# Performance work log

Hardware: AMD Instinct MI355X
Metric: run time of the kernel (lower is better)

## Reference

```python
import jax, jax.numpy as jnp
import numpy as np

B, D, K, NC, R = 32768, 512, 64, 64, 8
TRANSPORT_EPS = 1e-3
TAU_MIN = 0.01
TAU_DENOM_MIN = 1e-3
SCALE = 0.02


def setup_inputs() -> dict:
    key = jax.random.key(0)
    ks = jax.random.split(key, 8)
    f = jnp.float32
    return {
        "z": jax.random.normal(ks[0], (B, D), f),
        "w_z": jax.random.normal(ks[1], (K, D), f) * SCALE,          # q_z_proj weight
        "b_z": jnp.zeros((K,), f),                                     # q_z_proj bias
        "g_out": jax.random.normal(ks[2], (R, K), f) * SCALE,         # q_gamma_out
        "g_u": jax.random.normal(ks[3], (R, D), f) * SCALE,           # q_gamma_u
        "g_v": jax.random.normal(ks[4], (R, D), f) * SCALE,           # q_gamma_v
        "chart_queries": jax.random.normal(ks[5], (NC, K), f) * SCALE,
        "w_t": jax.random.normal(ks[6], (K * K, D), f) * SCALE,      # transport_proj weight
    }


def reference(z, w_z, b_z, g_out, g_u, g_v, chart_queries, w_t):
    # query: linear + low-rank gamma term (z_u * z_v) @ g_out
    q = z @ w_z.T + b_z                                # [B, K]
    q = q + ((z @ g_u.T) * (z @ g_v.T)) @ g_out        # [B, K]

    # Wilson-line transport: Cayley transform of a skew-symmetric matrix
    skew = (z @ w_t.T).reshape(-1, K, K)               # [B, K, K]
    skew = 0.5 * (skew - jnp.swapaxes(skew, 1, 2))
    eye = (1.0 + TRANSPORT_EPS) * jnp.eye(K, dtype=z.dtype)
    u = jnp.linalg.solve(eye + 0.5 * skew, eye[None, :, :] - 0.5 * skew)  # [B, K, K]

    keys = jnp.einsum('bij,nj->bni', u, chart_queries)  # [B, NC, K]
    scores = jnp.einsum('bnk,bk->bn', keys, q)          # [B, NC]

    # metric-aware temperature
    r2 = jnp.sum(z * z, axis=-1)
    denom = jnp.maximum(1.0 - r2, TAU_DENOM_MIN)
    tau = jnp.maximum(jnp.sqrt(jnp.asarray(K, z.dtype)) * denom / 2.0, TAU_MIN)

    router_weights = jax.nn.softmax(scores / tau[:, None], axis=-1)
    K_chart = jnp.argmax(router_weights, axis=-1)
    return router_weights, K_chart
```

## Files before the change

### kernel.cpp

```cpp
#include <hip/hip_runtime.h>
#include <cstdint>
#include <cstddef>
#include <cmath>

#define B_N   32768
#define D_DIM 512
#define NC_N  64
#define NTRI  2016
#define NP    2176
#define Q0    2016
#define U0    2080
#define V0    2088
#define KP    1536
#define KT_N  24
#define TEPS  1e-3f
#define SC1   0x1.0p-22f

typedef unsigned short u16;
typedef _Float16 f16;
typedef __attribute__((ext_vector_type(8))) _Float16 f16x8;
typedef __attribute__((ext_vector_type(4))) float f32x4;
typedef __attribute__((ext_vector_type(2))) float f32x2;

__device__ __forceinline__ u16 h_of(float x) { f16 h = (f16)x; return *reinterpret_cast<u16*>(&h); }
__device__ __forceinline__ float f_of_h(u16 u) { f16 h = *reinterpret_cast<f16*>(&u); return (float)h; }
__device__ __forceinline__ float rdlane(float x, int k) {
    return __int_as_float(__builtin_amdgcn_readlane(__float_as_int(x), k));
}
__device__ __forceinline__ float frcp(float x) {
    float r = __builtin_amdgcn_rcpf(x);
    return r * fmaf(-x, r, 2.0f);
}

__device__ __forceinline__ void split2(float x, u16& h, u16& l) {
    float s = x * 2048.0f;
    h = h_of(s);
    l = h_of(s - f_of_h(h));
}

__global__ __launch_bounds__(256) void prep_w_kernel(
    const float* __restrict__ wt, const float* __restrict__ wz,
    const float* __restrict__ gu, const float* __restrict__ gv,
    u16* __restrict__ dst)
{
    int t = blockIdx.x * 256 + threadIdx.x;
    if (t >= NP * 128) return;
    int row = t >> 7;
    int c4  = (t & 127) << 2;
    float4 v = make_float4(0.f, 0.f, 0.f, 0.f);
    if (row < NTRI) {
        int p = row;
        int i = (int)((127.0 - sqrt(16129.0 - 8.0 * (double)p)) * 0.5);
        if (i < 0) i = 0; if (i > 62) i = 62;
        while (i > 0 && (i * (127 - i)) / 2 > p) --i;
        while (((i + 1) * (126 - i)) / 2 <= p) ++i;
        int j = p - (i * (127 - i)) / 2 + i + 1;
        float4 a = *(const float4*)(wt + (size_t)(j * 64 + i) * 512 + c4);
        float4 b = *(const float4*)(wt + (size_t)(i * 64 + j) * 512 + c4);
        v.x = 0.25f * (a.x - b.x);
        v.y = 0.25f * (a.y - b.y);
        v.z = 0.25f * (a.z - b.z);
        v.w = 0.25f * (a.w - b.w);
    }
    else if (row < U0)        v = *(const float4*)(wz + (size_t)(row - Q0) * 512 + c4);
    else if (row < V0)        v = *(const float4*)(gu + (size_t)(row - U0) * 512 + c4);
    else if (row < V0 + 8)    v = *(const float4*)(gv + (size_t)(row - V0) * 512 + c4);
    ushort4 hv, lv;
    split2(v.x, hv.x, lv.x); split2(v.y, hv.y, lv.y);
    split2(v.z, hv.z, lv.z); split2(v.w, hv.w, lv.w);
    u16* base = dst + (size_t)row * KP + c4;
    *(ushort4*)(base)        = hv;
    *(ushort4*)(base + 512)  = lv;
    *(ushort4*)(base + 1024) = hv;
}

__global__ __launch_bounds__(256) void prep_z_kernel(
    const float* __restrict__ z, u16* __restrict__ dst, int chunkStart, int CB)
{
    int t = blockIdx.x * 256 + threadIdx.x;
    if (t >= CB * 128) return;
    int row = t >> 7;
    int c4  = (t & 127) << 2;
    float4 v = *(const float4*)(z + (size_t)(chunkStart + row) * 512 + c4);
    ushort4 hv, lv;
    split2(v.x, hv.x, lv.x); split2(v.y, hv.y, lv.y);
    split2(v.z, hv.z, lv.z); split2(v.w, hv.w, lv.w);
    u16* base = dst + (size_t)row * KP + c4;
    *(ushort4*)(base)        = hv;
    *(ushort4*)(base + 512)  = hv;
    *(ushort4*)(base + 1024) = lv;
}

__global__ __launch_bounds__(256) void gemm_kernel(
    const u16* __restrict__ A, const u16* __restrict__ Bw, float* __restrict__ C)
{
    __shared__ alignas(16) u16 As[128 * 64];
    __shared__ alignas(16) u16 Bs[128 * 64];
    const int t    = threadIdx.x;
    const int lane = t & 63;
    const int w    = t >> 6;
    const int wr   = w >> 1, wc = w & 1;

    const int nwg = gridDim.x * gridDim.y;
    int flat = blockIdx.y * gridDim.x + blockIdx.x;
    if ((nwg & 7) == 0) {
        const int cpx = nwg >> 3;
        flat = (flat & 7) * cpx + (flat >> 3);
    }
    const int bx = flat % gridDim.x;
    const int by = flat / gridDim.x;
    const size_t m0 = (size_t)by * 128;
    const size_t n0 = (size_t)bx * 128;

    const char* Ab = (const char*)A  + (m0 + (size_t)(t >> 3)) * (KP * 2) + (size_t)(t & 7) * 16;
    const char* Bb = (const char*)Bw + (n0 + (size_t)(t >> 3)) * (KP * 2) + (size_t)(t & 7) * 16;
    char* AsB = (char*)&As[0];
    char* BsB = (char*)&Bs[0];

    f32x4 acc[4][4];
    #pragma unroll
    for (int i = 0; i < 4; ++i)
        #pragma unroll
        for (int j = 0; j < 4; ++j)
            acc[i][j] = (f32x4){0.f, 0.f, 0.f, 0.f};

    const int lr = lane & 15;
    const int lk = (lane >> 4) * 8;

    #pragma unroll 1
    for (int kt = 0; kt < KT_N; ++kt) {
        __syncthreads();
        const size_t koff = (size_t)kt * 128;
        #pragma unroll
        for (int cc = 0; cc < 4; ++cc) {
            __builtin_amdgcn_global_load_lds(
                (const __attribute__((address_space(1))) unsigned int*)(Ab + (size_t)cc * (32 * KP * 2) + koff),
                (__attribute__((address_space(3))) unsigned int*)(AsB + cc * 4096 + w * 1024),
                16, 0, 0);
            __builtin_amdgcn_global_load_lds(
                (const __attribute__((address_space(1))) unsigned int*)(Bb + (size_t)cc * (32 * KP * 2) + koff),
                (__attribute__((address_space(3))) unsigned int*)(BsB + cc * 4096 + w * 1024),
                16, 0, 0);
        }
        asm volatile("s_waitcnt vmcnt(0)" ::: "memory");
        __syncthreads();
        #pragma unroll
        for (int kk = 0; kk < 64; kk += 32) {
            f16x8 af[4], bf[4];
            #pragma unroll
            for (int i = 0; i < 4; ++i) {
                af[i] = *(const f16x8*)&As[(wr * 64 + i * 16 + lr) * 64 + kk + lk];
                bf[i] = *(const f16x8*)&Bs[(wc * 64 + i * 16 + lr) * 64 + kk + lk];
            }
            #pragma unroll
            for (int i = 0; i < 4; ++i)
                #pragma unroll
                for (int j = 0; j < 4; ++j)
                    acc[i][j] = __builtin_amdgcn_mfma_f32_16x16x32_f16(af[i], bf[j], acc[i][j], 0, 0, 0);
        }
    }
    const int fq = lane >> 4;
    const int fr = lane & 15;
    #pragma unroll
    for (int i = 0; i < 4; ++i) {
        #pragma unroll
        for (int j = 0; j < 4; ++j) {
            size_t crow = m0 + (size_t)(wr * 64 + i * 16 + fq * 4);
            size_t ccol = n0 + (size_t)(wc * 64 + j * 16 + fr);
            #pragma unroll
            for (int r = 0; r < 4; ++r)
                __builtin_nontemporal_store(acc[i][j][r] * SC1, &C[(crow + r) * NP + ccol]);
        }
    }
}

__global__ __launch_bounds__(256) void solve_kernel(
    const float* __restrict__ z, const float* __restrict__ bz,
    const float* __restrict__ gout, const float* __restrict__ cq,
    const float* __restrict__ G, float* __restrict__ rw, float* __restrict__ kc,
    int chunkStart)
{
    const int tid  = threadIdx.x;
    const int lane = tid & 63;
    const int smp  = tid >> 6;
    const int sl   = (blockIdx.x << 2) + smp;
    const size_t s = (size_t)chunkStart + sl;
    const float c  = 1.0f + TEPS;

    __shared__ alignas(16) float Vs[4][2048];

    const float* Grow = G + (size_t)sl * NP;

    const float4* G4 = (const float4*)Grow;
    float4* Vw = (float4*)&Vs[smp][0];
    #pragma unroll
    for (int it = 0; it < 8; ++it) {
        int idx = it * 64 + lane;
        if (idx < NTRI / 4) Vw[idx] = G4[idx];
    }

    const float4* zr = (const float4*)(z + s * 512);
    float4 za = zr[lane];
    float4 zb = zr[64 + lane];
    float r2 = za.x * za.x + za.y * za.y + za.z * za.z + za.w * za.w
             + zb.x * zb.x + zb.y * zb.y + zb.z * zb.z + zb.w * zb.w;
    #pragma unroll
    for (int o = 32; o; o >>= 1) r2 += __shfl_xor(r2, o);

    float qv = bz[lane] + Grow[Q0 + lane];
    #pragma unroll
    for (int r = 0; r < 8; ++r) {
        float a = Grow[U0 + r];
        float b = Grow[V0 + r];
        qv = fmaf(a * b, gout[r * 64 + lane], qv);
    }
    const float qorig = qv;

    const int ibase = (lane * (127 - lane)) / 2 - lane - 1;
    f32x2 m2[32];
    #pragma unroll
    for (int j = 0; j < 64; ++j) {
        const int jbase = (j * (127 - j)) / 2 - j - 1;
        int addr = (j > lane) ? (ibase + j) : (jbase + lane);
        addr = (j == lane) ? 0 : addr;
        float v = Vs[smp][addr];
        float val = (j > lane) ? v : -v;
        val = (j == lane) ? 0.0f : val;
        if (j & 1) m2[j >> 1].y = val; else m2[j >> 1].x = val;
    }

    float myinv = 0.0f;
    #pragma unroll
    for (int k = 0; k < 64; ++k) {
        const int kp = k >> 1;
        const float mk = (k & 1) ? m2[kp].y : m2[kp].x;
        float piv = rdlane(mk, k) + c;
        float inv = frcp(piv);
        bool isk = (lane == k);
        float f = isk ? 0.0f : mk * inv;
        myinv = isk ? inv : myinv;
        const float nf = -f;
        const f32x2 nf2 = {nf, nf};
        qv = fmaf(nf, rdlane(qv, k), qv);
        if ((k & 1) == 0) {
            m2[kp].y = fmaf(nf, rdlane(m2[kp].y, k), m2[kp].y);
        }
        #pragma unroll
        for (int p = kp + 1; p < 32; ++p) {
            f32x2 bc;
            bc.x = rdlane(m2[p].x, k);
            bc.y = rdlane(m2[p].y, k);
            m2[p] = __builtin_elementwise_fma(nf2, bc, m2[p]);
        }
        if (k & 1) m2[kp].y = f; else m2[kp].x = f;
    }
    float y = qv * myinv;

    double rr_d = (double)qorig - (double)c * (double)y;
    #pragma unroll
    for (int j = 0; j < 64; ++j) {
        const int jbase = (j * (127 - j)) / 2 - j - 1;
        int addr = (j > lane) ? (ibase + j) : (jbase + lane);
        addr = (j == lane) ? 0 : addr;
        float v = Vs[smp][addr];
        float val = (j > lane) ? v : -v;
        val = (j == lane) ? 0.0f : val;
        rr_d -= (double)val * (double)rdlane(y, j);
    }
    float rf = (float)rr_d;
    #pragma unroll
    for (int k = 0; k < 64; ++k) {
        const float mk = (k & 1) ? m2[k >> 1].y : m2[k >> 1].x;
        rf = fmaf(-mk, rdlane(rf, k), rf);
    }
    y = fmaf(rf, myinv, y);

    const float v = 2.0f * c * y - qorig;

    float sc = 0.0f;
    const float4* cr = (const float4*)(cq + (size_t)lane * 64);
    #pragma unroll
    for (int j4 = 0; j4 < 16; ++j4) {
        float4 c4 = cr[j4];
        sc = fmaf(c4.x, rdlane(v, 4 * j4 + 0), sc);
        sc = fmaf(c4.y, rdlane(v, 4 * j4 + 1), sc);
        sc = fmaf(c4.z, rdlane(v, 4 * j4 + 2), sc);
        sc = fmaf(c4.w, rdlane(v, 4 * j4 + 3), sc);
    }

    float denom = fmaxf(1.0f - r2, 1e-3f);
    float tau   = fmaxf(4.0f * denom, 0.01f);
    float logit = sc * frcp(tau);
    float mx = logit;
    #pragma unroll
    for (int o = 32; o; o >>= 1) mx = fmaxf(mx, __shfl_xor(mx, o));
    float e = __expf(logit - mx);
    float sum = e;
    #pragma unroll
    for (int o = 32; o; o >>= 1) sum += __shfl_xor(sum, o);
    rw[s * 64 + lane] = e * frcp(sum);

    unsigned long long bal = __ballot(logit == mx);
    if (lane == 0) kc[s] = (float)(__ffsll(bal) - 1);
}

extern "C" void kernel_launch(void* const* d_in, const int* in_sizes, int n_in,
                              void* d_out, int out_size, void* d_ws, size_t ws_size,
                              hipStream_t stream)
{
    const float* z    = (const float*)d_in[0];
    const float* wz   = (const float*)d_in[1];
    const float* bz   = (const float*)d_in[2];
    const float* gout = (const float*)d_in[3];
    const float* gu   = (const float*)d_in[4];
    const float* gv   = (const float*)d_in[5];
    const float* cq   = (const float*)d_in[6];
    const float* wt   = (const float*)d_in[7];

    float* rw = (float*)d_out;
    float* kc = rw + (size_t)B_N * NC_N;

    const size_t whl_b = (size_t)NP * KP * 2;
    int CB = 128;
    const int cands[9] = {32768, 16384, 8192, 4096, 2048, 1024, 512, 256, 128};
    for (int i = 0; i < 9; ++i) {
        size_t need = whl_b + (size_t)cands[i] * ((size_t)KP * 2 + (size_t)NP * 4);
        if (need <= ws_size) { CB = cands[i]; break; }
    }

    u16*   w_hl = (u16*)d_ws;
    u16*   z_hl = (u16*)((char*)d_ws + whl_b);
    float* G    = (float*)((char*)d_ws + whl_b + (size_t)CB * KP * 2);

    prep_w_kernel<<<NP / 2, 256, 0, stream>>>(wt, wz, gu, gv, w_hl);
    for (int cs = 0; cs < B_N; cs += CB) {
        prep_z_kernel<<<CB / 2, 256, 0, stream>>>(z, z_hl, cs, CB);
        gemm_kernel<<<dim3(NP / 128, CB / 128), 256, 0, stream>>>(z_hl, w_hl, G);
        solve_kernel<<<CB / 4, 256, 0, stream>>>(z, bz, gout, cq, G, rw, kc, cs);
    }
}
```

Measured before the change: 697.0 us.

## Use 256x256 double-buffered swizzled-LDS GEMM tiles with 512 threads

The GEMM kernel moves from 128x128 tiles with 256 threads and single-buffered LDS to 256x256 tiles with 8 waves. LDS is double-buffered: the next k-tile is loaded through global_load_lds while MFMAs run on the current one, and the LDS layout is XOR-swizzled to avoid bank conflicts. NP is padded from 2176 to 2304 so it divides evenly into 256-wide tiles, which adds some wasted columns of work and a larger G buffer. The minimum chunk size also rises to 256 rows.

```diff
diff --git a/kernel.cpp b/kernel.cpp
--- a/kernel.cpp
+++ b/kernel.cpp
@@ -7,7 +7,7 @@
 #define D_DIM 512
 #define NC_N  64
 #define NTRI  2016
-#define NP    2176
+#define NP    2304
 #define Q0    2016
 #define U0    2080
 #define V0    2088
@@ -31,7 +31,6 @@
     float r = __builtin_amdgcn_rcpf(x);
     return r * fmaf(-x, r, 2.0f);
 }
-
 __device__ __forceinline__ void split2(float x, u16& h, u16& l) {
     float s = x * 2048.0f;
     h = h_of(s);
@@ -91,15 +90,19 @@
     *(ushort4*)(base + 1024) = lv;
 }
 
-__global__ __launch_bounds__(256) void gemm_kernel(
+__global__ __launch_bounds__(512, 2) void gemm_kernel(
     const u16* __restrict__ A, const u16* __restrict__ Bw, float* __restrict__ C)
 {
-    __shared__ alignas(16) u16 As[128 * 64];
-    __shared__ alignas(16) u16 Bs[128 * 64];
-    const int t    = threadIdx.x;
-    const int lane = t & 63;
-    const int w    = t >> 6;
-    const int wr   = w >> 1, wc = w & 1;
+    __shared__ alignas(16) u16 Ab[2][256 * 64];
+    __shared__ alignas(16) u16 Bb[2][256 * 64];
+    const int tid  = threadIdx.x;
+    const int lane = tid & 63;
+    const int wid  = tid >> 6;
+    const int wr   = wid >> 2;
+    const int wc   = wid & 3;
+    const int lr16 = lane & 15;
+    const int hk16 = (lane >> 4) * 16;
+    const int sw   = (lr16 & 7) << 4;
 
     const int nwg = gridDim.x * gridDim.y;
     int flat = blockIdx.y * gridDim.x + blockIdx.x;
@@ -109,67 +112,102 @@
     }
     const int bx = flat % gridDim.x;
     const int by = flat / gridDim.x;
-    const size_t m0 = (size_t)by * 128;
-    const size_t n0 = (size_t)bx * 128;
-
-    const char* Ab = (const char*)A  + (m0 + (size_t)(t >> 3)) * (KP * 2) + (size_t)(t & 7) * 16;
-    const char* Bb = (const char*)Bw + (n0 + (size_t)(t >> 3)) * (KP * 2) + (size_t)(t & 7) * 16;
-    char* AsB = (char*)&As[0];
-    char* BsB = (char*)&Bs[0];
-
-    f32x4 acc[4][4];
-    #pragma unroll
-    for (int i = 0; i < 4; ++i)
+    const size_t m0 = (size_t)by * 256;
+    const size_t n0 = (size_t)bx * 256;
+
+    const int rT  = tid >> 3;
+    const int cT  = (tid & 7) * 16;
+    const int cSw = cT ^ ((rT & 7) << 4);
+
+    const char* Ag = (const char*)A  + (m0 + rT) * (size_t)(KP * 2) + cSw;
+    const char* Bg = (const char*)Bw + (n0 + rT) * (size_t)(KP * 2) + cSw;
+    char* AsB = (char*)&Ab[0][0];
+    char* BsB = (char*)&Bb[0][0];
+    const int dstoff = rT * 128 + cT;
+
+#define STAGE(MATG, MATL, bufi, kt, h, s) \
+    __builtin_amdgcn_global_load_lds( \
+        (const __attribute__((address_space(1))) unsigned int*)((MATG) + (size_t)((h)*128 + (s)*64) * (KP*2) + (size_t)(kt)*128), \
+        (__attribute__((address_space(3))) unsigned int*)((MATL) + (bufi)*32768 + ((h)*128 + (s)*64)*128 + dstoff), \
+        16, 0, 0)
+
+    f32x4 acc[8][4];
+    #pragma unroll
+    for (int i = 0; i < 8; ++i)
         #pragma unroll
         for (int j = 0; j < 4; ++j)
             acc[i][j] = (f32x4){0.f, 0.f, 0.f, 0.f};
 
-    const int lr = lane & 15;
-    const int lk = (lane >> 4) * 8;
-
+    STAGE(Ag, AsB, 0, 0, 0, 0); STAGE(Ag, AsB, 0, 0, 0, 1);
+    STAGE(Ag, AsB, 0, 0, 1, 0); STAGE(Ag, AsB, 0, 0, 1, 1);
+    STAGE(Bg, BsB, 0, 0, 0, 0); STAGE(Bg, BsB, 0, 0, 0, 1);
+    STAGE(Bg, BsB, 0, 0, 1, 0); STAGE(Bg, BsB, 0, 0, 1, 1);
+    asm volatile("s_waitcnt vmcnt(0)" ::: "memory");
+    __builtin_amdgcn_s_barrier();
+
+    int cur = 0;
     #pragma unroll 1
     for (int kt = 0; kt < KT_N; ++kt) {
-        __syncthreads();
-        const size_t koff = (size_t)kt * 128;
-        #pragma unroll
-        for (int cc = 0; cc < 4; ++cc) {
-            __builtin_amdgcn_global_load_lds(
-                (const __attribute__((address_space(1))) unsigned int*)(Ab + (size_t)cc * (32 * KP * 2) + koff),
-                (__attribute__((address_space(3))) unsigned int*)(AsB + cc * 4096 + w * 1024),
-                16, 0, 0);
-            __builtin_amdgcn_global_load_lds(
-                (const __attribute__((address_space(1))) unsigned int*)(Bb + (size_t)cc * (32 * KP * 2) + koff),
-                (__attribute__((address_space(3))) unsigned int*)(BsB + cc * 4096 + w * 1024),
-                16, 0, 0);
+        const int nb = cur ^ 1;
+        const bool pf = (kt + 1 < KT_N);
+        const char* Ac = AsB + cur * 32768;
+        const char* Bc = BsB + cur * 32768;
+        f16x8 bf[4][2];
+        #pragma unroll
+        for (int nf = 0; nf < 4; ++nf) {
+            const int row = wc * 64 + nf * 16 + lr16;
+            #pragma unroll
+            for (int kh = 0; kh < 2; ++kh)
+                bf[nf][kh] = *(const f16x8*)(Bc + row * 128 + ((kh * 64 + hk16) ^ sw));
         }
-        asm volatile("s_waitcnt vmcnt(0)" ::: "memory");
-        __syncthreads();
-        #pragma unroll
-        for (int kk = 0; kk < 64; kk += 32) {
-            f16x8 af[4], bf[4];
+        #pragma unroll
+        for (int ph = 0; ph < 4; ++ph) {
+            f16x8 a0[2], a1[2];
+            const int r0 = wr * 128 + (2 * ph) * 16 + lr16;
             #pragma unroll
-            for (int i = 0; i < 4; ++i) {
-                af[i] = *(const f16x8*)&As[(wr * 64 + i * 16 + lr) * 64 + kk + lk];
-                bf[i] = *(const f16x8*)&Bs[(wc * 64 + i * 16 + lr) * 64 + kk + lk];
+            for (int kh = 0; kh < 2; ++kh) {
+                const int cb = (kh * 64 + hk16) ^ sw;
+                a0[kh] = *(const f16x8*)(Ac + r0 * 128 + cb);
+                a1[kh] = *(const f16x8*)(Ac + (r0 + 16) * 128 + cb);
             }
+            if (pf) {
+                if (ph == 0) { STAGE(Ag, AsB, nb, kt + 1, 0, 0); STAGE(Ag, AsB, nb, kt + 1, 0, 1); }
+                if (ph == 1) { STAGE(Ag, AsB, nb, kt + 1, 1, 0); STAGE(Ag, AsB, nb, kt + 1, 1, 1); }
+                if (ph == 2) { STAGE(Bg, BsB, nb, kt + 1, 0, 0); STAGE(Bg, BsB, nb, kt + 1, 0, 1); }
+                if (ph == 3) { STAGE(Bg, BsB, nb, kt + 1, 1, 0); STAGE(Bg, BsB, nb, kt + 1, 1, 1); }
+            }
+            __builtin_amdgcn_s_barrier();
+            asm volatile("s_waitcnt lgkmcnt(0)" ::: "memory");
+            __builtin_amdgcn_sched_barrier(0);
+            __builtin_amdgcn_s_setprio(1);
             #pragma unroll
-            for (int i = 0; i < 4; ++i)
+            for (int nf = 0; nf < 4; ++nf) {
                 #pragma unroll
-                for (int j = 0; j < 4; ++j)
-                    acc[i][j] = __builtin_amdgcn_mfma_f32_16x16x32_f16(af[i], bf[j], acc[i][j], 0, 0, 0);
+                for (int kh = 0; kh < 2; ++kh) {
+                    acc[2 * ph    ][nf] = __builtin_amdgcn_mfma_f32_16x16x32_f16(a0[kh], bf[nf][kh], acc[2 * ph    ][nf], 0, 0, 0);
+                    acc[2 * ph + 1][nf] = __builtin_amdgcn_mfma_f32_16x16x32_f16(a1[kh], bf[nf][kh], acc[2 * ph + 1][nf], 0, 0, 0);
+                }
+            }
+            __builtin_amdgcn_s_setprio(0);
+            if (ph == 3)
+                asm volatile("s_waitcnt vmcnt(0)" ::: "memory");
+            __builtin_amdgcn_s_barrier();
         }
-    }
+        cur ^= 1;
+    }
+#undef STAGE
+
     const int fq = lane >> 4;
     const int fr = lane & 15;
     #pragma unroll
-    for (int i = 0; i < 4; ++i) {
-        #pragma unroll
-        for (int j = 0; j < 4; ++j) {
-            size_t crow = m0 + (size_t)(wr * 64 + i * 16 + fq * 4);
-            size_t ccol = n0 + (size_t)(wc * 64 + j * 16 + fr);
+    for (int mf = 0; mf < 8; ++mf) {
+        #pragma unroll
+        for (int nf = 0; nf < 4; ++nf) {
+            size_t crow = m0 + (size_t)(wr * 128 + mf * 16 + fq * 4);
+            size_t ccol = n0 + (size_t)(wc * 64 + nf * 16 + fr);
             #pragma unroll
             for (int r = 0; r < 4; ++r)
-                __builtin_nontemporal_store(acc[i][j][r] * SC1, &C[(crow + r) * NP + ccol]);
+                __builtin_nontemporal_store(acc[mf][nf][r] * SC1, &C[(crow + r) * NP + ccol]);
         }
     }
 }
@@ -242,9 +280,8 @@
         const float nf = -f;
         const f32x2 nf2 = {nf, nf};
         qv = fmaf(nf, rdlane(qv, k), qv);
-        if ((k & 1) == 0) {
+        if ((k & 1) == 0)
             m2[kp].y = fmaf(nf, rdlane(m2[kp].y, k), m2[kp].y);
-        }
         #pragma unroll
         for (int p = kp + 1; p < 32; ++p) {
             f32x2 bc;
@@ -321,9 +358,9 @@
     float* kc = rw + (size_t)B_N * NC_N;
 
     const size_t whl_b = (size_t)NP * KP * 2;
-    int CB = 128;
-    const int cands[9] = {32768, 16384, 8192, 4096, 2048, 1024, 512, 256, 128};
-    for (int i = 0; i < 9; ++i) {
+    int CB = 256;
+    const int cands[8] = {32768, 16384, 8192, 4096, 2048, 1024, 512, 256};
+    for (int i = 0; i < 8; ++i) {
         size_t need = whl_b + (size_t)cands[i] * ((size_t)KP * 2 + (size_t)NP * 4);
         if (need <= ws_size) { CB = cands[i]; break; }
     }
@@ -335,7 +372,7 @@
     prep_w_kernel<<<NP / 2, 256, 0, stream>>>(wt, wz, gu, gv, w_hl);
     for (int cs = 0; cs < B_N; cs += CB) {
         prep_z_kernel<<<CB / 2, 256, 0, stream>>>(z, z_hl, cs, CB);
-        gemm_kernel<<<dim3(NP / 128, CB / 128), 256, 0, stream>>>(z_hl, w_hl, G);
+        gemm_kernel<<<dim3(NP / 256, CB / 256), 512, 0, stream>>>(z_hl, w_hl, G);
         solve_kernel<<<CB / 4, 256, 0, stream>>>(z, bz, gout, cq, G, rw, kc, cs);
     }
 }
```

Result: slower. 717.2 us (+2.9%).

## Fuse chunked GEMM with previous chunk's solve in one launch, double-buffered

Applied to the files above, without the earlier changes.

Merges the GEMM for chunk i and the Cayley-solve for chunk i-1 into one kernel whose blocks branch by index, with two G buffers so both stages run concurrently on the GPU. It also converts all of z to split-fp16 form in one up-front launch and caps the chunk size at 4096. The goal is to overlap the memory/MFMA-bound GEMM with the latency-bound solve and cut per-chunk launch overhead. In exchange it needs more workspace (the full z_hl plus two G buffers) and shares one smem allocation between the two roles, which may limit occupancy.

```diff
diff --git a/kernel.cpp b/kernel.cpp
--- a/kernel.cpp
+++ b/kernel.cpp
@@ -31,7 +31,6 @@
     float r = __builtin_amdgcn_rcpf(x);
     return r * fmaf(-x, r, 2.0f);
 }
-
 __device__ __forceinline__ void split2(float x, u16& h, u16& l) {
     float s = x * 2048.0f;
     h = h_of(s);
@@ -75,13 +74,12 @@
 }
 
 __global__ __launch_bounds__(256) void prep_z_kernel(
-    const float* __restrict__ z, u16* __restrict__ dst, int chunkStart, int CB)
+    const float* __restrict__ z, u16* __restrict__ dst)
 {
     int t = blockIdx.x * 256 + threadIdx.x;
-    if (t >= CB * 128) return;
     int row = t >> 7;
     int c4  = (t & 127) << 2;
-    float4 v = *(const float4*)(z + (size_t)(chunkStart + row) * 512 + c4);
+    float4 v = *(const float4*)(z + (size_t)row * 512 + c4);
     ushort4 hv, lv;
     split2(v.x, hv.x, lv.x); split2(v.y, hv.y, lv.y);
     split2(v.z, hv.z, lv.z); split2(v.w, hv.w, lv.w);
@@ -91,31 +89,31 @@
     *(ushort4*)(base + 1024) = lv;
 }
 
-__global__ __launch_bounds__(256) void gemm_kernel(
-    const u16* __restrict__ A, const u16* __restrict__ Bw, float* __restrict__ C)
-{
-    __shared__ alignas(16) u16 As[128 * 64];
-    __shared__ alignas(16) u16 Bs[128 * 64];
+__device__ __forceinline__ void gemm_body(
+    char* smem, const u16* __restrict__ A, const u16* __restrict__ Bw,
+    float* __restrict__ C, int gemmBlocks, int bidx)
+{
+    u16* As = (u16*)smem;
+    u16* Bs = (u16*)(smem + 16384);
     const int t    = threadIdx.x;
     const int lane = t & 63;
     const int w    = t >> 6;
     const int wr   = w >> 1, wc = w & 1;
 
-    const int nwg = gridDim.x * gridDim.y;
-    int flat = blockIdx.y * gridDim.x + blockIdx.x;
-    if ((nwg & 7) == 0) {
-        const int cpx = nwg >> 3;
+    int flat = bidx;
+    if ((gemmBlocks & 7) == 0) {
+        const int cpx = gemmBlocks >> 3;
         flat = (flat & 7) * cpx + (flat >> 3);
     }
-    const int bx = flat % gridDim.x;
-    const int by = flat / gridDim.x;
+    const int bx = flat % (NP / 128);
+    const int by = flat / (NP / 128);
     const size_t m0 = (size_t)by * 128;
     const size_t n0 = (size_t)bx * 128;
 
     const char* Ab = (const char*)A  + (m0 + (size_t)(t >> 3)) * (KP * 2) + (size_t)(t & 7) * 16;
     const char* Bb = (const char*)Bw + (n0 + (size_t)(t >> 3)) * (KP * 2) + (size_t)(t & 7) * 16;
-    char* AsB = (char*)&As[0];
-    char* BsB = (char*)&Bs[0];
+    char* AsB = (char*)As;
+    char* BsB = (char*)Bs;
 
     f32x4 acc[4][4];
     #pragma unroll
@@ -174,20 +172,20 @@
     }
 }
 
-__global__ __launch_bounds__(256) void solve_kernel(
-    const float* __restrict__ z, const float* __restrict__ bz,
+__device__ __forceinline__ void solve_body(
+    char* smem, const float* __restrict__ z, const float* __restrict__ bz,
     const float* __restrict__ gout, const float* __restrict__ cq,
     const float* __restrict__ G, float* __restrict__ rw, float* __restrict__ kc,
-    int chunkStart)
-{
+    int solveStart, int sb)
+{
+    float (*Vs)[2048] = (float (*)[2048])smem;
+
     const int tid  = threadIdx.x;
     const int lane = tid & 63;
     const int smp  = tid >> 6;
-    const int sl   = (blockIdx.x << 2) + smp;
-    const size_t s = (size_t)chunkStart + sl;
+    const int sl   = (sb << 2) + smp;
+    const size_t s = (size_t)solveStart + sl;
     const float c  = 1.0f + TEPS;
-
-    __shared__ alignas(16) float Vs[4][2048];
 
     const float* Grow = G + (size_t)sl * NP;
 
@@ -242,9 +240,8 @@
         const float nf = -f;
         const f32x2 nf2 = {nf, nf};
         qv = fmaf(nf, rdlane(qv, k), qv);
-        if ((k & 1) == 0) {
+        if ((k & 1) == 0)
             m2[kp].y = fmaf(nf, rdlane(m2[kp].y, k), m2[kp].y);
-        }
         #pragma unroll
         for (int p = kp + 1; p < 32; ++p) {
             f32x2 bc;
@@ -304,6 +301,32 @@
     if (lane == 0) kc[s] = (float)(__ffsll(bal) - 1);
 }
 
+__global__ __launch_bounds__(256) void fused_kernel(
+    const u16* __restrict__ A, const u16* __restrict__ Bw, float* __restrict__ Cg,
+    int gemmBlocks,
+    const float* __restrict__ z, const float* __restrict__ bz,
+    const float* __restrict__ gout, const float* __restrict__ cq,
+    const float* __restrict__ Gp, float* __restrict__ rw, float* __restrict__ kc,
+    int solveStart)
+{
+    __shared__ alignas(16) char smem[32768];
+    if ((int)blockIdx.x < gemmBlocks)
+        gemm_body(smem, A, Bw, Cg, gemmBlocks, blockIdx.x);
+    else
+        solve_body(smem, z, bz, gout, cq, Gp, rw, kc, solveStart,
+                   blockIdx.x - gemmBlocks);
+}
+
+__global__ __launch_bounds__(256) void solve_kernel(
+    const float* __restrict__ z, const float* __restrict__ bz,
+    const float* __restrict__ gout, const float* __restrict__ cq,
+    const float* __restrict__ G, float* __restrict__ rw, float* __restrict__ kc,
+    int solveStart)
+{
+    __shared__ alignas(16) char smem[32768];
+    solve_body(smem, z, bz, gout, cq, G, rw, kc, solveStart, blockIdx.x);
+}
+
 extern "C" void kernel_launch(void* const* d_in, const int* in_sizes, int n_in,
                               void* d_out, int out_size, void* d_ws, size_t ws_size,
                               hipStream_t stream)
@@ -321,21 +344,39 @@
     float* kc = rw + (size_t)B_N * NC_N;
 
     const size_t whl_b = (size_t)NP * KP * 2;
-    int CB = 128;
-    const int cands[9] = {32768, 16384, 8192, 4096, 2048, 1024, 512, 256, 128};
-    for (int i = 0; i < 9; ++i) {
-        size_t need = whl_b + (size_t)cands[i] * ((size_t)KP * 2 + (size_t)NP * 4);
-        if (need <= ws_size) { CB = cands[i]; break; }
-    }
+    const size_t zhl_b = (size_t)B_N * KP * 2;
+
+    int CB = 4096;
+    while (CB > 512) {
+        size_t need = whl_b + zhl_b + 2 * (size_t)CB * NP * 4;
+        if (need <= ws_size) break;
+        CB >>= 1;
+    }
+    const int nchunks = B_N / CB;
+    const int GB = (CB / 128) * (NP / 128);
+    const int SBLK = CB / 4;
 
     u16*   w_hl = (u16*)d_ws;
     u16*   z_hl = (u16*)((char*)d_ws + whl_b);
-    float* G    = (float*)((char*)d_ws + whl_b + (size_t)CB * KP * 2);
+    float* G0   = (float*)((char*)d_ws + whl_b + zhl_b);
+    float* G1   = G0 + (size_t)CB * NP;
 
     prep_w_kernel<<<NP / 2, 256, 0, stream>>>(wt, wz, gu, gv, w_hl);
-    for (int cs = 0; cs < B_N; cs += CB) {
-        prep_z_kernel<<<CB / 2, 256, 0, stream>>>(z, z_hl, cs, CB);
-        gemm_kernel<<<dim3(NP / 128, CB / 128), 256, 0, stream>>>(z_hl, w_hl, G);
-        solve_kernel<<<CB / 4, 256, 0, stream>>>(z, bz, gout, cq, G, rw, kc, cs);
-    }
-}
+    prep_z_kernel<<<B_N / 2, 256, 0, stream>>>(z, z_hl);
+
+    for (int i = 0; i < nchunks; ++i) {
+        float* Gc = (i & 1) ? G1 : G0;
+        const float* Gp = (i & 1) ? G0 : G1;
+        const u16* Ac = z_hl + (size_t)i * CB * KP;
+        if (i == 0) {
+            fused_kernel<<<GB, 256, 0, stream>>>(
+                Ac, w_hl, Gc, GB, z, bz, gout, cq, Gp, rw, kc, 0);
+        } else {
+            fused_kernel<<<GB + SBLK, 256, 0, stream>>>(
+                Ac, w_hl, Gc, GB, z, bz, gout, cq, Gp, rw, kc, (i - 1) * CB);
+        }
+    }
+    const float* Glast = ((nchunks - 1) & 1) ? G1 : G0;
+    solve_kernel<<<SBLK, 256, 0, stream>>>(
+        z, bz, gout, cq, Glast, rw, kc, (nchunks - 1) * CB);
+}
```

New measurement: 1.367 ms. 96.1% more time.
